# Kernel tuning notes

Hardware: AMD Instinct MI355X
Metric: run time of the kernel (lower is better)

Reference implementation:

```python
import jax, jax.numpy as jnp
import numpy as np

# ---- fixed config (matches A_Sp_P4CNN cfg with n_channels=32) ----
C = 32          # n_channels
B = 32          # batch
H = W = 48      # input spatial size
KS = 3          # main conv kernel
SPK = 7         # spatial-attention kernel
EPS = 2e-5      # BatchNorm eps
NG = 4          # p4 rotation group size (n_grid)
SAME7 = [(SPK // 2, SPK // 2)] * 2  # 'same' padding for attention convs


def _conv2d(x, w, padding):
    return jax.lax.conv_general_dilated(
        x, w, window_strides=(1, 1), padding=padding,
        dimension_numbers=('NCHW', 'OIHW', 'NCHW'))


def _rot(w, r):
    # rotate kernel spatially by r*90 deg (p4 group action on Z2 kernels)
    return jnp.rot90(w, k=r, axes=(-2, -1))


def _gg_rot(w, r):
    # p4 action on a GG kernel [O,I,4,k,k]: spatial rotation + cyclic shift of
    # the input-rotation axis
    return jnp.roll(_rot(w, r), shift=r, axis=2)


def _lift_conv(x, w, padding):
    # lifting conv Z2 -> p4: x [B,Ci,H,W], w [Co,Ci,k,k] -> [B,Co,4,H',W']
    return jnp.stack([_conv2d(x, _rot(w, r), padding) for r in range(NG)], axis=2)


def _gg_conv(x, w, padding):
    # group conv p4 -> p4: x [B,Ci,4,H,W], w [Co,Ci,4,k,k] -> [B,Co,4,H',W']
    b, ci, g, h, ww = x.shape
    xf = x.reshape(b, ci * g, h, ww)
    outs = []
    for r in range(NG):
        wr = _gg_rot(w, r).reshape(w.shape[0], ci * g, w.shape[-2], w.shape[-1])
        outs.append(_conv2d(xf, wr, padding))
    return jnp.stack(outs, axis=2)


def _sp_att_rng(x, aw):
    # CBAM-style spatial attention lifted to p4: [B,Ci,H,W] -> [B,1,4,H,W]
    a = jnp.concatenate([jnp.mean(x, 1, keepdims=True),
                         jnp.max(x, 1, keepdims=True)], axis=1)
    return jax.nn.sigmoid(_lift_conv(a, aw, SAME7))


def _sp_att_gg(x, aw):
    # spatial attention on a p4 feature map: [B,Ci,4,H,W] -> [B,1,4,H,W]
    a = jnp.concatenate([jnp.mean(x, 1, keepdims=True),
                         jnp.max(x, 1, keepdims=True)], axis=1)
    return jax.nn.sigmoid(_gg_conv(a, aw, SAME7))


def _att_conv_rng(x, w, bias, aw):
    # attentive lifting conv: per output rotation r, modulate the input with the
    # r-th spatial attention map, then convolve with the r-rotated kernel
    att = _sp_att_rng(x, aw)  # [B,1,4,H,W]
    outs = [_conv2d(att[:, :, r] * x, _rot(w, r), 'VALID') for r in range(NG)]
    return jnp.stack(outs, axis=2) + bias[None, :, None, None, None]


def _att_conv_gg(x, w, bias, aw):
    # attentive group conv: attention broadcast over channels + input rotations
    att = _sp_att_gg(x, aw)  # [B,1,4,H,W]
    b, ci, g, h, ww = x.shape
    outs = []
    for r in range(NG):
        xr = (att[:, :, r][:, :, None] * x).reshape(b, ci * g, h, ww)
        wr = _gg_rot(w, r).reshape(w.shape[0], ci * g, KS, KS)
        outs.append(_conv2d(xr, wr, 'VALID'))
    return jnp.stack(outs, axis=2) + bias[None, :, None, None, None]


def _bn3d(x, gamma, beta):
    # BatchNorm3d over [B,C,4,H,W]: per-channel stats over (B,4,H,W) (training-mode math)
    m = jnp.mean(x, axis=(0, 2, 3, 4), keepdims=True)
    v = jnp.var(x, axis=(0, 2, 3, 4), keepdims=True)
    return gamma[None, :, None, None, None] * (x - m) * jax.lax.rsqrt(v + EPS) \
        + beta[None, :, None, None, None]


def _max_pool2(x):
    # max_pooling_Rn: 2x2/2 spatial max pool on [B,C,4,H,W]
    return jax.lax.reduce_window(x, -jnp.inf, jax.lax.max,
                                 (1, 1, 1, 2, 2), (1, 1, 1, 2, 2), 'VALID')


def setup_inputs() -> dict:
    key = jax.random.key(0)
    ks = jax.random.split(key, 40)
    sd = 0.1
    inp = {'x': jax.random.normal(ks[0], (B, 1, H, W), dtype=jnp.float32)}
    # c1: lifting conv 1 -> C
    inp['w1'] = jax.random.normal(ks[1], (C, 1, KS, KS), dtype=jnp.float32) * sd
    inp['b1'] = jnp.zeros((C,), jnp.float32)
    inp['aw1'] = jax.random.normal(ks[2], (1, 2, SPK, SPK), dtype=jnp.float32) * sd
    # c2..c6: GG convs C -> C
    for i in range(2, 7):
        inp[f'w{i}'] = jax.random.normal(ks[3 * i], (C, C, NG, KS, KS), dtype=jnp.float32) * sd
        inp[f'b{i}'] = jnp.zeros((C,), jnp.float32)
        inp[f'aw{i}'] = jax.random.normal(ks[3 * i + 1], (1, 2, NG, SPK, SPK), dtype=jnp.float32) * sd
    # c7: GG conv C -> 10 (classifier)
    inp['w7'] = jax.random.normal(ks[30], (10, C, NG, KS, KS), dtype=jnp.float32) * sd
    inp['b7'] = jnp.zeros((10,), jnp.float32)
    inp['aw7'] = jax.random.normal(ks[31], (1, 2, NG, SPK, SPK), dtype=jnp.float32) * sd
    # BatchNorm3d affine params bn1..bn6
    for i in range(1, 7):
        inp[f'g{i}'] = jnp.ones((C,), jnp.float32)
        inp[f'be{i}'] = jnp.zeros((C,), jnp.float32)
    return inp


def reference(x, w1, b1, aw1, w2, b2, aw2, w3, b3, aw3, w4, b4, aw4,
              w5, b5, aw5, w6, b6, aw6, w7, b7, aw7,
              g1, be1, g2, be2, g3, be3, g4, be4, g5, be5, g6, be6):
    # dropout is identity in eval-mode reference
    out = jax.nn.relu(_bn3d(_att_conv_rng(x, w1, b1, aw1), g1, be1))
    out = jax.nn.relu(_bn3d(_att_conv_gg(out, w2, b2, aw2), g2, be2))
    out = _max_pool2(out)
    out = jax.nn.relu(_bn3d(_att_conv_gg(out, w3, b3, aw3), g3, be3))
    out = jax.nn.relu(_bn3d(_att_conv_gg(out, w4, b4, aw4), g4, be4))
    out = jax.nn.relu(_bn3d(_att_conv_gg(out, w5, b5, aw5), g5, be5))
    out = jax.nn.relu(_bn3d(_att_conv_gg(out, w6, b6, aw6), g6, be6))
    out = _att_conv_gg(out, w7, b7, aw7)  # [B,10,4,h,w]
    out = jnp.max(out, axis=2)            # pool over rotation group (dim=-3)
    out = jnp.mean(out, axis=(2, 3))      # adaptive_avg_pool2d(1) + view
    return out                             # [B,10]
```

## Files before the change

### kernel.cpp

```cpp
#include <hip/hip_runtime.h>
#include <cstddef>

#define DINL static __device__ __forceinline__

typedef __attribute__((ext_vector_type(4))) float f4v;
typedef __attribute__((ext_vector_type(8))) short bh8;
typedef __attribute__((ext_vector_type(4))) unsigned short us4;

DINL void rot_src(int r, int K, int i, int j, int& si, int& sj) {
  switch (r & 3) {
    case 0:  si = i;       sj = j;       break;
    case 1:  si = j;       sj = K-1-i;   break;
    case 2:  si = K-1-i;   sj = K-1-j;   break;
    default: si = K-1-j;   sj = i;       break;
  }
}

DINL float sigmoidf(float s) { return 1.f / (1.f + __expf(-s)); }

DINL unsigned short f2bf(float f) {
  unsigned u = __builtin_bit_cast(unsigned, f);
  u += 0x7fffu + ((u >> 16) & 1u);
  return (unsigned short)(u >> 16);
}
DINL float bf2f(unsigned short h) {
  unsigned u = ((unsigned)h) << 16;
  return __builtin_bit_cast(float, u);
}

DINL void bn_finalize_par(const float* __restrict__ partl,
                          const float* __restrict__ gamma, const float* __restrict__ beta,
                          float* st, float* l1, float* l2, int npix, int tid) {
  if (tid < 256) {
    int c = tid & 31, grp = tid >> 5;
    float s1 = 0.f, s2 = 0.f;
    #pragma unroll
    for (int k = 0; k < 8; ++k) {
      int bk = grp * 8 + k;
      s1 += partl[bk * 128 + c];
      s2 += partl[bk * 128 + 64 + c];
    }
    l1[tid] = s1; l2[tid] = s2;
  }
  __syncthreads();
  if (tid < 32) {
    float a = 0.f, q = 0.f;
    #pragma unroll
    for (int k = 0; k < 8; ++k) { a += l1[k * 32 + tid]; q += l2[k * 32 + tid]; }
    float N = 4.f * (float)npix;
    float m = a / N;
    float v = q / N - m * m;
    float inv = rsqrtf(v + 2e-5f);
    float sc = gamma[tid] * inv;
    st[tid] = sc;
    st[32 + tid] = beta[tid] - m * sc;
  }
  __syncthreads();
}

__global__ void __launch_bounds__(256)
k_prep_att(const float* __restrict__ w2, const float* __restrict__ w3,
           const float* __restrict__ w4, const float* __restrict__ w5,
           const float* __restrict__ w6, const float* __restrict__ w7,
           unsigned short* __restrict__ wrot,
           const float* __restrict__ x, const float* __restrict__ aw1,
           float* __restrict__ att, float* __restrict__ part) {
  __shared__ float wsum[4][49];
  __shared__ float xs[12 * 48];
  int bid = blockIdx.x;
  if (bid < 3168) {
    int idx = bid * 256 + threadIdx.x;
    const float* w; int OM, O, base;
    if (idx < 737280) {
      int L = idx / 147456; base = L * 147456; OM = 2; O = 32;
      w = (L == 0) ? w2 : (L == 1) ? w3 : (L == 2) ? w4 : (L == 3) ? w5 : w6;
    } else { base = 737280; OM = 1; O = 10; w = w7; }
    int local = idx - base;
    int j = local & 7; int t = local >> 3;
    int lanei = t & 63; t >>= 6;
    int mi = t % OM; t /= OM;
    int ks = t & 3; t >>= 2;
    int tap = t % 9; int r = t / 9;
    int n = lanei & 15, q = lanei >> 4;
    int o = mi * 16 + n;
    int ci = q * 8 + j;
    int gs = (ks - r) & 3;
    int ky = tap / 3, kx = tap % 3;
    int si, sj; rot_src(r, 3, ky, kx, si, sj);
    float val = (o < O) ? w[((o * 32 + ci) * 4 + gs) * 9 + si * 3 + sj] : 0.f;
    wrot[idx] = f2bf(val);
  } else if (bid < 4192) {
    const int H = 48, HW = H * H, BH = 6, NB = 8;
    int id = bid - 3168;
    int band = id % NB; int t = id / NB;
    int r = t & 3; int b = t >> 2;
    int row0 = band * BH;
    int base = row0 - 3;
    for (int i = threadIdx.x; i < 196; i += 256) {
      int rr = i / 49; int tt = i % 49;
      int ky = tt / 7, kx = tt % 7;
      int si, sj; rot_src(rr, 7, ky, kx, si, sj);
      wsum[rr][tt] = aw1[si * 7 + sj] + aw1[49 + si * 7 + sj];
    }
    const float* xb = x + b * HW;
    for (int i = threadIdx.x; i < 12 * 48; i += 256) {
      int rr = base + i / 48;
      xs[i] = ((unsigned)rr < (unsigned)H) ? xb[rr * H + (i % 48)] : 0.f;
    }
    __syncthreads();
    for (int i = threadIdx.x; i < BH * H; i += 256) {
      int yh = row0 + i / H; int xw = i % H;
      float s = 0.f;
      for (int ky = 0; ky < 7; ++ky) {
        int y = yh + ky - 3;
        if ((unsigned)y >= (unsigned)H) continue;
        for (int kx = 0; kx < 7; ++kx) {
          int xx = xw + kx - 3;
          if ((unsigned)xx >= (unsigned)H) continue;
          s += xs[(y - base) * H + xx] * wsum[r][ky * 7 + kx];
        }
      }
      att[(size_t)(b * 4 + r) * HW + yh * H + xw] = sigmoidf(s);
    }
  } else {
    int zb = bid - 4192;
    int off = zb * 2048 + threadIdx.x;
    #pragma unroll
    for (int k = 0; k < 8; ++k) part[off + k * 256] = 0.f;
  }
}

__global__ void __launch_bounds__(256)
k_conv_lift(const float* __restrict__ x, const float* __restrict__ att,
            const float* __restrict__ w, const float* __restrict__ bias,
            unsigned short* __restrict__ y, float* __restrict__ partl) {
  const int HO = 46;
  __shared__ float xs[3 * 48];
  __shared__ float as[4][3 * 48];
  __shared__ float wsm[288];
  __shared__ float bs[32];
  __shared__ float bnred[64];
  int id = blockIdx.x;
  int yo = id % HO; int b = id / HO;

  for (int i = threadIdx.x; i < 144; i += 256)
    xs[i] = x[b * 2304 + (yo + i / 48) * 48 + (i % 48)];
  for (int i = threadIdx.x; i < 576; i += 256) {
    int r = i / 144; int rem = i % 144;
    as[r][rem] = att[(b * 4 + r) * 2304 + (yo + rem / 48) * 48 + (rem % 48)];
  }
  for (int i = threadIdx.x; i < 288; i += 256) wsm[i] = w[i];
  if (threadIdx.x < 32) bs[threadIdx.x] = bias[threadIdx.x];
  if (threadIdx.x < 64) bnred[threadIdx.x] = 0.f;
  __syncthreads();

  int o = threadIdx.x & 31;
  int cl = threadIdx.x >> 5;
  float wreg[9];
  #pragma unroll
  for (int i = 0; i < 9; ++i) wreg[i] = wsm[o * 9 + i];
  float bv = bs[o];
  float sacc = 0.f, qacc = 0.f;

  for (int c8 = 0; c8 < 6; ++c8) {
    int col = c8 * 8 + cl;
    if (col < HO) {
      float xv[9];
      #pragma unroll
      for (int ky = 0; ky < 3; ++ky)
        #pragma unroll
        for (int kx = 0; kx < 3; ++kx)
          xv[ky * 3 + kx] = xs[ky * 48 + col + kx];
      unsigned short* yp = y + ((size_t)b * 2116 + yo * HO + col) * 128 + o;
      #pragma unroll
      for (int r = 0; r < 4; ++r) {
        float acc = bv;
        #pragma unroll
        for (int ky = 0; ky < 3; ++ky)
          #pragma unroll
          for (int kx = 0; kx < 3; ++kx) {
            int si, sj; rot_src(r, 3, ky, kx, si, sj);
            acc = fmaf(as[r][ky * 48 + col + kx] * xv[ky * 3 + kx], wreg[si * 3 + sj], acc);
          }
        yp[r * 32] = f2bf(acc);
        sacc += acc; qacc += acc * acc;
      }
    }
  }
  atomicAdd(&bnred[o], sacc);
  atomicAdd(&bnred[32 + o], qacc);
  __syncthreads();
  if (threadIdx.x < 64) {
    int bucket = blockIdx.x & 63;
    int c = threadIdx.x & 31;
    int off = (threadIdx.x < 32) ? c : (64 + c);
    atomicAdd(&partl[bucket * 128 + off], bnred[threadIdx.x]);
  }
}

template<int H, int OM, int O, int OSTR, bool BNS>
__global__ void __launch_bounds__(256)
k_conv_mfma(const unsigned short* __restrict__ xn, const float* __restrict__ att,
            const unsigned short* __restrict__ wl, const float* __restrict__ bias,
            unsigned short* __restrict__ y, float* __restrict__ partl) {
  constexpr int HO = H - 2, HW = H * H;
  constexpr int TR = 8, TC = 16, WR = TR + 2, WC = TC + 2, CGH = 68;
  constexpr int NRT = (HO + TR - 1) / TR, NCT = (HO + TC - 1) / TC;
  constexpr int NPIX = WR * WC;
  constexpr int NCH = NPIX * 8;
  constexpr int NST = (NCH + 255) / 256;
  __shared__ __align__(16) unsigned short xa[2][NPIX * CGH];
  __shared__ float bnred[128];

  int id = blockIdx.x;
  int slot = id & 7; int k = id >> 3;
  int tile = k % (NRT * NCT); k /= (NRT * NCT);
  int r = k & 3; int bhi = k >> 2;
  int b = bhi * 8 + slot;
  int rt = tile / NCT, ct = tile % NCT;
  int row0 = rt * TR, c0 = ct * TC;

  const unsigned short* xb = xn + (size_t)b * HW * 128;
  const float* ab = att + (size_t)(b * 4 + r) * HW;

  int tid = threadIdx.x;
  int lane = tid & 63;
  int wv = tid >> 6;
  int n = lane & 15, quad = lane >> 4;

  f4v acc[OM][2];
  #pragma unroll
  for (int mi = 0; mi < OM; ++mi)
    #pragma unroll
    for (int ri = 0; ri < 2; ++ri) {
      acc[mi][ri][0] = 0.f; acc[mi][ri][1] = 0.f;
      acc[mi][ri][2] = 0.f; acc[mi][ri][3] = 0.f;
    }

  const bh8* wa = (const bh8*)wl + (size_t)r * 9 * 4 * OM * 64 + lane;

  bh8 wqa[4], wqb[4];
  auto wload = [&](int s) {
    int hh = s / 18, tt = s % 18, tp = tt >> 1, kk = tt & 1, ks2 = hh * 2 + kk;
    wqa[s & 3] = wa[(size_t)((tp * 4 + ks2) * OM + 0) * 64];
    if constexpr (OM == 2)
      wqb[s & 3] = wa[(size_t)((tp * 4 + ks2) * OM + 1) * 64];
  };

  bh8 sx[NST]; float sa[NST];
  auto issue = [&](int half) {
    #pragma unroll
    for (int i = 0; i < NST; ++i) {
      int u = tid + i * 256;
      if (i + 1 < NST || u < NCH) {
        int ch = u & 7; int pix = u >> 3;
        int wr = pix / WC, wc = pix % WC;
        int row = row0 + wr; if (row > H - 1) row = H - 1;
        int col = c0 + wc;  if (col > H - 1) col = H - 1;
        int p = row * H + col;
        sx[i] = *(const bh8*)(xb + (size_t)p * 128 + half * 64 + ch * 8);
        sa[i] = ab[p];
      }
    }
  };
  auto wlds = [&](int half) {
    #pragma unroll
    for (int i = 0; i < NST; ++i) {
      int u = tid + i * 256;
      if (i + 1 < NST || u < NCH) {
        int ch = u & 7; int pix = u >> 3;
        bh8 v;
        #pragma unroll
        for (int j2 = 0; j2 < 8; ++j2)
          v[j2] = (short)f2bf(bf2f((unsigned short)sx[i][j2]) * sa[i]);
        *(bh8*)&xa[half][pix * CGH + ch * 8] = v;
      }
    }
  };
  auto mfma_half = [&](int half) {
    #pragma unroll
    for (int t = 0; t < 18; ++t) {
      const int s = half * 18 + t;
      bh8 a0 = wqa[s & 3];
      bh8 a1;
      if constexpr (OM == 2) a1 = wqb[s & 3];
      if (s + 4 < 36) wload(s + 4);
      const int tap = t >> 1, kl = t & 1;
      const int ky = tap / 3, kx = tap % 3;
      int pb0 = ((2 * wv + ky) * WC + n + kx) * CGH;
      int pb1 = pb0 + WC * CGH;
      bh8 b0 = *(const bh8*)&xa[half][pb0 + kl * 32 + quad * 8];
      bh8 b1 = *(const bh8*)&xa[half][pb1 + kl * 32 + quad * 8];
      acc[0][0] = __builtin_amdgcn_mfma_f32_16x16x32_bf16(a0, b0, acc[0][0], 0, 0, 0);
      acc[0][1] = __builtin_amdgcn_mfma_f32_16x16x32_bf16(a0, b1, acc[0][1], 0, 0, 0);
      if constexpr (OM == 2) {
        acc[1][0] = __builtin_amdgcn_mfma_f32_16x16x32_bf16(a1, b0, acc[1][0], 0, 0, 0);
        acc[1][1] = __builtin_amdgcn_mfma_f32_16x16x32_bf16(a1, b1, acc[1][1], 0, 0, 0);
      }
    }
  };

  wload(0); wload(1); wload(2); wload(3);
  issue(0);
  wlds(0);
  __syncthreads();
  issue(1);
  mfma_half(0);
  wlds(1);
  __syncthreads();
  mfma_half(1);

  float sv[OM * 4], qv[OM * 4];
  #pragma unroll
  for (int e = 0; e < OM * 4; ++e) { sv[e] = 0.f; qv[e] = 0.f; }
  #pragma unroll
  for (int mi = 0; mi < OM; ++mi)
    #pragma unroll
    for (int ri = 0; ri < 2; ++ri) {
      int prow = row0 + 2 * wv + ri;
      int col = c0 + n;
      if (prow < HO && col < HO) {
        unsigned short* yp = y + ((size_t)b * HO * HO + prow * HO + col) * OSTR;
        int o0 = mi * 16 + quad * 4;
        f4v v = acc[mi][ri];
        if constexpr (O == 32) {
          us4 w4;
          #pragma unroll
          for (int reg = 0; reg < 4; ++reg) {
            float val = v[reg] + bias[o0 + reg];
            w4[reg] = f2bf(val);
            if constexpr (BNS) { sv[mi * 4 + reg] += val; qv[mi * 4 + reg] += val * val; }
          }
          *(us4*)(yp + r * 32 + o0) = w4;
        } else {
          #pragma unroll
          for (int reg = 0; reg < 4; ++reg) {
            int o = o0 + reg;
            if (o < O) yp[r * O + o] = f2bf(v[reg] + bias[o]);
          }
        }
      }
    }

  if constexpr (BNS) {
    #pragma unroll
    for (int e = 0; e < OM * 4; ++e) {
      #pragma unroll
      for (int off = 1; off < 16; off <<= 1) {
        sv[e] += __shfl_xor(sv[e], off);
        qv[e] += __shfl_xor(qv[e], off);
      }
    }
    if (threadIdx.x < 128) bnred[threadIdx.x] = 0.f;
    __syncthreads();
    if (n == 0) {
      #pragma unroll
      for (int e = 0; e < OM * 4; ++e) {
        int o = (e >> 2) * 16 + quad * 4 + (e & 3);
        atomicAdd(&bnred[o], sv[e]);
        atomicAdd(&bnred[64 + o], qv[e]);
      }
    }
    __syncthreads();
    if (threadIdx.x < 128)
      atomicAdd(&partl[(blockIdx.x & 63) * 128 + threadIdx.x], bnred[threadIdx.x]);
  }
}

template<int HIN, int HOUT, bool POOL>
__global__ void __launch_bounds__(256)
k_postA(const unsigned short* __restrict__ yr, const float* __restrict__ partl,
        const float* __restrict__ gamma, const float* __restrict__ beta,
        unsigned short* __restrict__ xn, unsigned short* __restrict__ amap) {
  __shared__ float st[64];
  __shared__ float l1[256], l2[256];
  bn_finalize_par(partl, gamma, beta, st, l1, l2, 32 * HIN * HIN, threadIdx.x);
  int idx = blockIdx.x * 256 + threadIdx.x;
  if (idx >= 32 * HOUT * HOUT * 4) return;
  int g = idx & 3; int p = idx >> 2;
  int col = p % HOUT; int t = p / HOUT;
  int row = t % HOUT; int b = t / HOUT;
  float sm = 0.f, mx = -1e30f;
  unsigned short* xp = xn + (size_t)p * 128 + g * 32;
  if constexpr (POOL) {
    const unsigned short* p00 =
        yr + ((size_t)b * HIN * HIN + (row * 2) * HIN + col * 2) * 128 + g * 32;
    #pragma unroll
    for (int k = 0; k < 4; ++k) {
      bh8 r0 = *(const bh8*)(p00 + k * 8);
      bh8 r1 = *(const bh8*)(p00 + 128 + k * 8);
      bh8 r2 = *(const bh8*)(p00 + (size_t)HIN * 128 + k * 8);
      bh8 r3 = *(const bh8*)(p00 + (size_t)(HIN + 1) * 128 + k * 8);
      bh8 w;
      #pragma unroll
      for (int e = 0; e < 8; ++e) {
        float sc = st[k * 8 + e], sh = st[32 + k * 8 + e];
        float a0 = fmaxf(fmaf(bf2f((unsigned short)r0[e]), sc, sh), 0.f);
        float a1 = fmaxf(fmaf(bf2f((unsigned short)r1[e]), sc, sh), 0.f);
        float a2 = fmaxf(fmaf(bf2f((unsigned short)r2[e]), sc, sh), 0.f);
        float a3 = fmaxf(fmaf(bf2f((unsigned short)r3[e]), sc, sh), 0.f);
        float val = fmaxf(fmaxf(a0, a1), fmaxf(a2, a3));
        w[e] = (short)f2bf(val);
        sm += val; mx = fmaxf(mx, val);
      }
      *(bh8*)(xp + k * 8) = w;
    }
  } else {
    const unsigned short* yp = yr + (size_t)p * 128 + g * 32;
    #pragma unroll
    for (int k = 0; k < 4; ++k) {
      bh8 raw = *(const bh8*)(yp + k * 8);
      bh8 w;
      #pragma unroll
      for (int e = 0; e < 8; ++e) {
        float v = fmaxf(fmaf(bf2f((unsigned short)raw[e]), st[k * 8 + e], st[32 + k * 8 + e]), 0.f);
        w[e] = (short)f2bf(v);
        sm += v;
        mx = fmaxf(mx, v);
      }
      *(bh8*)(xp + k * 8) = w;
    }
  }
  amap[(size_t)p * 8 + g] = f2bf(sm * (1.f / 32.f));
  amap[(size_t)p * 8 + 4 + g] = f2bf(mx);
}

__global__ void __launch_bounds__(256)
k_att_gg(const unsigned short* __restrict__ amap, const float* __restrict__ aw,
         float* __restrict__ att, int h, int bh, int nb) {
  __shared__ float wsa[4][4][49], wsx[4][4][49];
  __shared__ __align__(16) unsigned short as_[5152];
  int id = blockIdx.x;
  int band = id % nb; int t = id / nb;
  int r = t & 3; int b = t >> 2;
  int row0 = band * bh;
  int base = row0 - 3;
  int nrows = bh + 6;
  for (int i = threadIdx.x; i < 784; i += 256) {
    int rr = i / 196; int rem = i % 196;
    int g = rem / 49; int tt = rem % 49;
    int ky = tt / 7, kx = tt % 7;
    int si, sj; rot_src(rr, 7, ky, kx, si, sj);
    int gs = (g - rr) & 3;
    wsa[rr][g][tt] = aw[gs * 49 + si * 7 + sj];
    wsx[rr][g][tt] = aw[(4 + gs) * 49 + si * 7 + sj];
  }
  int hw = h * h;
  const unsigned short* ab = amap + (size_t)b * hw * 8;
  int nch = nrows * h;
  for (int i = threadIdx.x; i < nch; i += 256) {
    int rr = base + i / h;
    bh8 v;
    if ((unsigned)rr < (unsigned)h) v = *(const bh8*)(ab + ((size_t)rr * h + (i % h)) * 8);
    else v = (bh8)(short)0;
    *(bh8*)&as_[i * 8] = v;
  }
  __syncthreads();
  for (int i = threadIdx.x; i < bh * h; i += 256) {
    int yh = row0 + i / h; int xw = i % h;
    if (yh >= h) continue;
    float s = 0.f;
    for (int ky = 0; ky < 7; ++ky) {
      int y = yh + ky - 3;
      if ((unsigned)y >= (unsigned)h) continue;
      for (int kx = 0; kx < 7; ++kx) {
        int xx = xw + kx - 3;
        if ((unsigned)xx >= (unsigned)h) continue;
        int tp = ky * 7 + kx;
        bh8 av = *(const bh8*)&as_[((y - base) * h + xx) * 8];
        #pragma unroll
        for (int g = 0; g < 4; ++g)
          s += bf2f((unsigned short)av[g]) * wsa[r][g][tp]
             + bf2f((unsigned short)av[4 + g]) * wsx[r][g][tp];
      }
    }
    att[(size_t)(b * 4 + r) * hw + yh * h + xw] = sigmoidf(s);
  }
}

__global__ void k_final(const unsigned short* __restrict__ y7, float* __restrict__ out) {
  int idx = blockIdx.x * blockDim.x + threadIdx.x;
  if (idx >= 320) return;
  int o = idx % 10; int b = idx / 10;
  const unsigned short* p = y7 + (size_t)b * 144 * 40;
  float s = 0.f;
  for (int sp = 0; sp < 144; ++sp) {
    const unsigned short* q = p + sp * 40 + o;
    float m = fmaxf(fmaxf(bf2f(q[0]), bf2f(q[10])), fmaxf(bf2f(q[20]), bf2f(q[30])));
    s += m;
  }
  out[idx] = s * (1.f / 144.f);
}


extern "C" void kernel_launch(void* const* d_in, const int* in_sizes, int n_in,
                              void* d_out, int out_size, void* d_ws, size_t ws_size,
                              hipStream_t stream) {
  (void)in_sizes; (void)n_in; (void)out_size; (void)ws_size;
  const float* x   = (const float*)d_in[0];
  const float* w1  = (const float*)d_in[1];
  const float* b1  = (const float*)d_in[2];
  const float* aw1 = (const float*)d_in[3];
  const float* W[6];  const float* BI[6]; const float* AW[6];
  for (int i = 0; i < 6; ++i) {
    W[i]  = (const float*)d_in[4 + 3 * i];
    BI[i] = (const float*)d_in[5 + 3 * i];
    AW[i] = (const float*)d_in[6 + 3 * i];
  }
  const float* G[6]; const float* BE[6];
  for (int i = 0; i < 6; ++i) {
    G[i]  = (const float*)d_in[22 + 2 * i];
    BE[i] = (const float*)d_in[23 + 2 * i];
  }
  float* out = (float*)d_out;

  float* ws = (float*)d_ws;
  unsigned short* YR = (unsigned short*)ws;
  unsigned short* XN = (unsigned short*)(ws + 4333568);
  unsigned short* AMAP = (unsigned short*)(ws + 8667136);
  float* ATT = ws + 8937984;
  unsigned short* WROT = (unsigned short*)(ws + 9232896);
  float* PART  = ws + 9638400;

  auto cdiv = [](int a, int b) { return (a + b - 1) / b; };
  float* PL[6];
  for (int i = 0; i < 6; ++i) PL[i] = PART + i * 8192;

  k_prep_att<<<dim3(4216), dim3(256), 0, stream>>>(
      W[0], W[1], W[2], W[3], W[4], W[5], WROT, x, aw1, ATT, PART);
  const unsigned short* WL[6];
  for (int i = 0; i < 5; ++i) WL[i] = WROT + i * 147456;
  WL[5] = WROT + 737280;

  k_conv_lift<<<dim3(32 * 46), dim3(256), 0, stream>>>(x, ATT, w1, b1, YR, PL[0]);
  k_postA<46, 46, false><<<dim3(cdiv(32 * 46 * 46 * 4, 256)), dim3(256), 0, stream>>>(YR, PL[0], G[0], BE[0], XN, AMAP);
  k_att_gg<<<dim3(32 * 4 * 6), dim3(256), 0, stream>>>(AMAP, AW[0], ATT, 46, 8, 6);
  k_conv_mfma<46, 2, 32, 128, true><<<dim3(128 * 6 * 3), dim3(256), 0, stream>>>(XN, ATT, WL[0], BI[0], YR, PL[1]);
  k_postA<44, 22, true><<<dim3(cdiv(32 * 22 * 22 * 4, 256)), dim3(256), 0, stream>>>(YR, PL[1], G[1], BE[1], XN, AMAP);
  k_att_gg<<<dim3(32 * 4 * 4), dim3(256), 0, stream>>>(AMAP, AW[1], ATT, 22, 6, 4);
  k_conv_mfma<22, 2, 32, 128, true><<<dim3(128 * 3 * 2), dim3(256), 0, stream>>>(XN, ATT, WL[1], BI[1], YR, PL[2]);
  k_postA<20, 20, false><<<dim3(cdiv(32 * 20 * 20 * 4, 256)), dim3(256), 0, stream>>>(YR, PL[2], G[2], BE[2], XN, AMAP);
  k_att_gg<<<dim3(32 * 4 * 4), dim3(256), 0, stream>>>(AMAP, AW[2], ATT, 20, 5, 4);
  k_conv_mfma<20, 2, 32, 128, true><<<dim3(128 * 3 * 2), dim3(256), 0, stream>>>(XN, ATT, WL[2], BI[2], YR, PL[3]);
  k_postA<18, 18, false><<<dim3(cdiv(32 * 18 * 18 * 4, 256)), dim3(256), 0, stream>>>(YR, PL[3], G[3], BE[3], XN, AMAP);
  k_att_gg<<<dim3(32 * 4 * 4), dim3(256), 0, stream>>>(AMAP, AW[3], ATT, 18, 5, 4);
  k_conv_mfma<18, 2, 32, 128, true><<<dim3(128 * 2 * 1), dim3(256), 0, stream>>>(XN, ATT, WL[3], BI[3], YR, PL[4]);
  k_postA<16, 16, false><<<dim3(cdiv(32 * 16 * 16 * 4, 256)), dim3(256), 0, stream>>>(YR, PL[4], G[4], BE[4], XN, AMAP);
  k_att_gg<<<dim3(32 * 4 * 4), dim3(256), 0, stream>>>(AMAP, AW[4], ATT, 16, 4, 4);
  k_conv_mfma<16, 2, 32, 128, true><<<dim3(128 * 2 * 1), dim3(256), 0, stream>>>(XN, ATT, WL[4], BI[4], YR, PL[5]);
  k_postA<14, 14, false><<<dim3(cdiv(32 * 14 * 14 * 4, 256)), dim3(256), 0, stream>>>(YR, PL[5], G[5], BE[5], XN, AMAP);
  k_att_gg<<<dim3(32 * 4 * 4), dim3(256), 0, stream>>>(AMAP, AW[5], ATT, 14, 4, 4);
  k_conv_mfma<14, 1, 10, 40, false><<<dim3(128 * 2 * 1), dim3(256), 0, stream>>>(XN, ATT, WL[5], BI[5], YR, nullptr);
  k_final<<<dim3(5), dim3(64), 0, stream>>>(YR, out);
}
```

Measured before the change: 365.2 us.

## Fuse spatial-attention 7x7 conv into MFMA group-conv kernel

Removes the separate k_att_gg launches and computes the sigmoid attention map for each conv tile's halo pixels inside k_conv_mfma, reading the mean/max map straight from global memory and keeping the rotated attention weights in shared memory. This eliminates six kernel launches and the ATT global write/read round trip. In exchange, halo pixels are recomputed redundantly across neighbouring tiles, and the 7x7 attention conv now sits serially before the first MFMA half, adding a sync and latency to every conv block.

```diff
diff --git a/kernel.cpp b/kernel.cpp
--- a/kernel.cpp
+++ b/kernel.cpp
@@ -200,7 +200,8 @@
 
 template<int H, int OM, int O, int OSTR, bool BNS>
 __global__ void __launch_bounds__(256)
-k_conv_mfma(const unsigned short* __restrict__ xn, const float* __restrict__ att,
+k_conv_mfma(const unsigned short* __restrict__ xn, const unsigned short* __restrict__ amap,
+            const float* __restrict__ aw,
             const unsigned short* __restrict__ wl, const float* __restrict__ bias,
             unsigned short* __restrict__ y, float* __restrict__ partl) {
   constexpr int HO = H - 2, HW = H * H;
@@ -211,6 +212,8 @@
   constexpr int NST = (NCH + 255) / 256;
   __shared__ __align__(16) unsigned short xa[2][NPIX * CGH];
   __shared__ float bnred[128];
+  __shared__ float wsa_l[4][49], wsx_l[4][49];
+  __shared__ float att_l[NPIX];
 
   int id = blockIdx.x;
   int slot = id & 7; int k = id >> 3;
@@ -221,7 +224,7 @@
   int row0 = rt * TR, c0 = ct * TC;
 
   const unsigned short* xb = xn + (size_t)b * HW * 128;
-  const float* ab = att + (size_t)(b * 4 + r) * HW;
+  const unsigned short* ab8 = amap + (size_t)b * HW * 8;
 
   int tid = threadIdx.x;
   int lane = tid & 63;
@@ -247,7 +250,7 @@
       wqb[s & 3] = wa[(size_t)((tp * 4 + ks2) * OM + 1) * 64];
   };
 
-  bh8 sx[NST]; float sa[NST];
+  bh8 sx[NST];
   auto issue = [&](int half) {
     #pragma unroll
     for (int i = 0; i < NST; ++i) {
@@ -259,7 +262,6 @@
         int col = c0 + wc;  if (col > H - 1) col = H - 1;
         int p = row * H + col;
         sx[i] = *(const bh8*)(xb + (size_t)p * 128 + half * 64 + ch * 8);
-        sa[i] = ab[p];
       }
     }
   };
@@ -269,10 +271,11 @@
       int u = tid + i * 256;
       if (i + 1 < NST || u < NCH) {
         int ch = u & 7; int pix = u >> 3;
+        float av = att_l[pix];
         bh8 v;
         #pragma unroll
         for (int j2 = 0; j2 < 8; ++j2)
-          v[j2] = (short)f2bf(bf2f((unsigned short)sx[i][j2]) * sa[i]);
+          v[j2] = (short)f2bf(bf2f((unsigned short)sx[i][j2]) * av);
         *(bh8*)&xa[half][pix * CGH + ch * 8] = v;
       }
     }
@@ -300,8 +303,40 @@
     }
   };
 
+  for (int i = tid; i < 196; i += 256) {
+    int g = i / 49; int t = i % 49;
+    int ky = t / 7, kx = t % 7;
+    int si, sj; rot_src(r, 7, ky, kx, si, sj);
+    int gs = (g - r) & 3;
+    wsa_l[g][t] = aw[gs * 49 + si * 7 + sj];
+    wsx_l[g][t] = aw[(4 + gs) * 49 + si * 7 + sj];
+  }
   wload(0); wload(1); wload(2); wload(3);
   issue(0);
+  __syncthreads();
+
+  if (tid < NPIX) {
+    int yh = row0 + tid / WC; if (yh > H - 1) yh = H - 1;
+    int xw = c0 + tid % WC;   if (xw > H - 1) xw = H - 1;
+    float s = 0.f;
+    for (int ky = 0; ky < 7; ++ky) {
+      int y = yh + ky - 3;
+      if ((unsigned)y >= (unsigned)H) continue;
+      for (int kx = 0; kx < 7; ++kx) {
+        int xx = xw + kx - 3;
+        if ((unsigned)xx >= (unsigned)H) continue;
+        int tp = ky * 7 + kx;
+        bh8 av = *(const bh8*)(ab8 + ((size_t)y * H + xx) * 8);
+        #pragma unroll
+        for (int g = 0; g < 4; ++g)
+          s += bf2f((unsigned short)av[g]) * wsa_l[g][tp]
+             + bf2f((unsigned short)av[4 + g]) * wsx_l[g][tp];
+      }
+    }
+    att_l[tid] = sigmoidf(s);
+  }
+  __syncthreads();
+
   wlds(0);
   __syncthreads();
   issue(1);
@@ -425,59 +460,6 @@
   amap[(size_t)p * 8 + 4 + g] = f2bf(mx);
 }
 
-__global__ void __launch_bounds__(256)
-k_att_gg(const unsigned short* __restrict__ amap, const float* __restrict__ aw,
-         float* __restrict__ att, int h, int bh, int nb) {
-  __shared__ float wsa[4][4][49], wsx[4][4][49];
-  __shared__ __align__(16) unsigned short as_[5152];
-  int id = blockIdx.x;
-  int band = id % nb; int t = id / nb;
-  int r = t & 3; int b = t >> 2;
-  int row0 = band * bh;
-  int base = row0 - 3;
-  int nrows = bh + 6;
-  for (int i = threadIdx.x; i < 784; i += 256) {
-    int rr = i / 196; int rem = i % 196;
-    int g = rem / 49; int tt = rem % 49;
-    int ky = tt / 7, kx = tt % 7;
-    int si, sj; rot_src(rr, 7, ky, kx, si, sj);
-    int gs = (g - rr) & 3;
-    wsa[rr][g][tt] = aw[gs * 49 + si * 7 + sj];
-    wsx[rr][g][tt] = aw[(4 + gs) * 49 + si * 7 + sj];
-  }
-  int hw = h * h;
-  const unsigned short* ab = amap + (size_t)b * hw * 8;
-  int nch = nrows * h;
-  for (int i = threadIdx.x; i < nch; i += 256) {
-    int rr = base + i / h;
-    bh8 v;
-    if ((unsigned)rr < (unsigned)h) v = *(const bh8*)(ab + ((size_t)rr * h + (i % h)) * 8);
-    else v = (bh8)(short)0;
-    *(bh8*)&as_[i * 8] = v;
-  }
-  __syncthreads();
-  for (int i = threadIdx.x; i < bh * h; i += 256) {
-    int yh = row0 + i / h; int xw = i % h;
-    if (yh >= h) continue;
-    float s = 0.f;
-    for (int ky = 0; ky < 7; ++ky) {
-      int y = yh + ky - 3;
-      if ((unsigned)y >= (unsigned)h) continue;
-      for (int kx = 0; kx < 7; ++kx) {
-        int xx = xw + kx - 3;
-        if ((unsigned)xx >= (unsigned)h) continue;
-        int tp = ky * 7 + kx;
-        bh8 av = *(const bh8*)&as_[((y - base) * h + xx) * 8];
-        #pragma unroll
-        for (int g = 0; g < 4; ++g)
-          s += bf2f((unsigned short)av[g]) * wsa[r][g][tp]
-             + bf2f((unsigned short)av[4 + g]) * wsx[r][g][tp];
-      }
-    }
-    att[(size_t)(b * 4 + r) * hw + yh * h + xw] = sigmoidf(s);
-  }
-}
-
 __global__ void k_final(const unsigned short* __restrict__ y7, float* __restrict__ out) {
   int idx = blockIdx.x * blockDim.x + threadIdx.x;
   if (idx >= 320) return;
@@ -534,22 +516,16 @@
 
   k_conv_lift<<<dim3(32 * 46), dim3(256), 0, stream>>>(x, ATT, w1, b1, YR, PL[0]);
   k_postA<46, 46, false><<<dim3(cdiv(32 * 46 * 46 * 4, 256)), dim3(256), 0, stream>>>(YR, PL[0], G[0], BE[0], XN, AMAP);
-  k_att_gg<<<dim3(32 * 4 * 6), dim3(256), 0, stream>>>(AMAP, AW[0], ATT, 46, 8, 6);
-  k_conv_mfma<46, 2, 32, 128, true><<<dim3(128 * 6 * 3), dim3(256), 0, stream>>>(XN, ATT, WL[0], BI[0], YR, PL[1]);
+  k_conv_mfma<46, 2, 32, 128, true><<<dim3(128 * 6 * 3), dim3(256), 0, stream>>>(XN, AMAP, AW[0], WL[0], BI[0], YR, PL[1]);
   k_postA<44, 22, true><<<dim3(cdiv(32 * 22 * 22 * 4, 256)), dim3(256), 0, stream>>>(YR, PL[1], G[1], BE[1], XN, AMAP);
-  k_att_gg<<<dim3(32 * 4 * 4), dim3(256), 0, stream>>>(AMAP, AW[1], ATT, 22, 6, 4);
-  k_conv_mfma<22, 2, 32, 128, true><<<dim3(128 * 3 * 2), dim3(256), 0, stream>>>(XN, ATT, WL[1], BI[1], YR, PL[2]);
+  k_conv_mfma<22, 2, 32, 128, true><<<dim3(128 * 3 * 2), dim3(256), 0, stream>>>(XN, AMAP, AW[1], WL[1], BI[1], YR, PL[2]);
   k_postA<20, 20, false><<<dim3(cdiv(32 * 20 * 20 * 4, 256)), dim3(256), 0, stream>>>(YR, PL[2], G[2], BE[2], XN, AMAP);
-  k_att_gg<<<dim3(32 * 4 * 4), dim3(256), 0, stream>>>(AMAP, AW[2], ATT, 20, 5, 4);
-  k_conv_mfma<20, 2, 32, 128, true><<<dim3(128 * 3 * 2), dim3(256), 0, stream>>>(XN, ATT, WL[2], BI[2], YR, PL[3]);
+  k_conv_mfma<20, 2, 32, 128, true><<<dim3(128 * 3 * 2), dim3(256), 0, stream>>>(XN, AMAP, AW[2], WL[2], BI[2], YR, PL[3]);
   k_postA<18, 18, false><<<dim3(cdiv(32 * 18 * 18 * 4, 256)), dim3(256), 0, stream>>>(YR, PL[3], G[3], BE[3], XN, AMAP);
-  k_att_gg<<<dim3(32 * 4 * 4), dim3(256), 0, stream>>>(AMAP, AW[3], ATT, 18, 5, 4);
-  k_conv_mfma<18, 2, 32, 128, true><<<dim3(128 * 2 * 1), dim3(256), 0, stream>>>(XN, ATT, WL[3], BI[3], YR, PL[4]);
+  k_conv_mfma<18, 2, 32, 128, true><<<dim3(128 * 2 * 1), dim3(256), 0, stream>>>(XN, AMAP, AW[3], WL[3], BI[3], YR, PL[4]);
   k_postA<16, 16, false><<<dim3(cdiv(32 * 16 * 16 * 4, 256)), dim3(256), 0, stream>>>(YR, PL[4], G[4], BE[4], XN, AMAP);
-  k_att_gg<<<dim3(32 * 4 * 4), dim3(256), 0, stream>>>(AMAP, AW[4], ATT, 16, 4, 4);
-  k_conv_mfma<16, 2, 32, 128, true><<<dim3(128 * 2 * 1), dim3(256), 0, stream>>>(XN, ATT, WL[4], BI[4], YR, PL[5]);
+  k_conv_mfma<16, 2, 32, 128, true><<<dim3(128 * 2 * 1), dim3(256), 0, stream>>>(XN, AMAP, AW[4], WL[4], BI[4], YR, PL[5]);
   k_postA<14, 14, false><<<dim3(cdiv(32 * 14 * 14 * 4, 256)), dim3(256), 0, stream>>>(YR, PL[5], G[5], BE[5], XN, AMAP);
-  k_att_gg<<<dim3(32 * 4 * 4), dim3(256), 0, stream>>>(AMAP, AW[5], ATT, 14, 4, 4);
-  k_conv_mfma<14, 1, 10, 40, false><<<dim3(128 * 2 * 1), dim3(256), 0, stream>>>(XN, ATT, WL[5], BI[5], YR, nullptr);
+  k_conv_mfma<14, 1, 10, 40, false><<<dim3(128 * 2 * 1), dim3(256), 0, stream>>>(XN, AMAP, AW[5], WL[5], BI[5], YR, nullptr);
   k_final<<<dim3(5), dim3(64), 0, stream>>>(YR, out);
 }
```

Result: no change. 361.8 us (-0.9%).
